# Kernel tuning notes

Hardware: AMD Instinct MI355X
Metric: run time of the kernel (lower is better)

The kernel has to match this reference:

```python
import jax, jax.numpy as jnp
import numpy as np

N_AREA = 10000
N_FEAT = 16
HID = 64
N_EDGE = 320000
BATCH = 64
EPS = 1e-5
SLOPE = 0.01  # F.leaky_relu default negative_slope


def _layer_norm(x, g, b):
    mu = jnp.mean(x, axis=-1, keepdims=True)
    var = jnp.mean(jnp.square(x - mu), axis=-1, keepdims=True)
    return (x - mu) * jax.lax.rsqrt(var + EPS) * g + b


def _leaky(x):
    return jnp.where(x >= 0, x, SLOPE * x)


def setup_inputs() -> dict:
    key = jax.random.key(0)
    ks = jax.random.split(key, 8)
    inp = {}
    inp["state"] = jax.random.normal(ks[0], (BATCH, N_AREA * N_FEAT), dtype=jnp.float32)
    inp["edge_index"] = jax.random.randint(ks[1], (2, N_EDGE), 0, N_AREA, dtype=jnp.int32)
    inp["batch_size"] = BATCH
    inp["rej_rate"] = jnp.zeros((1,), jnp.float32)
    inp["theta_value"] = jnp.zeros((1,), jnp.float32)
    inp["W1"] = jax.random.normal(ks[2], (N_FEAT, HID), jnp.float32) * 0.1
    inp["b1"] = jnp.zeros((HID,), jnp.float32)
    inp["W2"] = jax.random.normal(ks[3], (HID, HID), jnp.float32) * 0.1
    inp["b2"] = jnp.zeros((HID,), jnp.float32)
    inp["W3"] = jax.random.normal(ks[4], (HID, HID), jnp.float32) * 0.1
    inp["b3"] = jnp.zeros((HID,), jnp.float32)
    inp["g1"] = jnp.ones((HID,), jnp.float32)
    inp["be1"] = jnp.zeros((HID,), jnp.float32)
    inp["g3"] = jnp.ones((HID,), jnp.float32)
    inp["be3"] = jnp.zeros((HID,), jnp.float32)
    inp["Wf"] = jax.random.normal(ks[5], (HID, HID), jnp.float32) * 0.1
    inp["bf"] = jnp.zeros((HID,), jnp.float32)
    return inp


def reference(state, edge_index, batch_size, rej_rate, theta_value,
              W1, b1, W2, b2, W3, b3, g1, be1, g3, be3, Wf, bf):
    B = batch_size
    x = state.reshape(B, N_AREA, N_FEAT)
    # GCN normalization with self-loops (PyG GCNConv default)
    loops = jnp.arange(N_AREA, dtype=edge_index.dtype)
    src = jnp.concatenate([edge_index[0], loops])
    dst = jnp.concatenate([edge_index[1], loops])
    deg = jnp.zeros((N_AREA,), state.dtype).at[dst].add(1.0)
    dinv = jax.lax.rsqrt(jnp.maximum(deg, 1.0))  # deg >= 1 due to self-loops
    norm = dinv[src] * dinv[dst]  # [E+N]

    def conv(h, W, b):
        hw = h @ W                                  # [B, N, H]
        msg = hw[:, src, :] * norm[None, :, None]   # gather over sources
        out = jnp.zeros((B, N_AREA, W.shape[1]), hw.dtype).at[:, dst, :].add(msg)
        return out + b

    h1 = _leaky(_layer_norm(conv(x, W1, b1), g1, be1))
    h2 = _leaky(conv(h1, W2, b2)) + h1
    h3 = _leaky(_layer_norm(conv(h2, W3, b3), g3, be3)) + h1
    out = jnp.tanh(h3 @ Wf + bf)
    return out.reshape(B, -1)
```

## Files before the change

### kernel.cpp

```cpp
#include <hip/hip_runtime.h>
#include <hip/hip_fp16.h>
#include <cstdint>
#include <cstddef>

#define N_AREA 10000
#define N_FEAT 16
#define HID 64
#define BATCH 64
#define EPSL 1e-5f
#define SLOPE 0.01f
#define NCHUNK 157

typedef float fv4 __attribute__((ext_vector_type(4)));

__device__ __forceinline__ float lrelu(float x) { return x >= 0.f ? x : SLOPE * x; }
__device__ __forceinline__ float tanh_fast(float x) {
    float t = __expf(2.0f * x);
    return 1.0f - 2.0f / (t + 1.0f);
}
__device__ __forceinline__ float2 h2f2(unsigned u) {
    return __half22float2(*reinterpret_cast<const __half2*>(&u));
}
__device__ __forceinline__ unsigned f2h2(float a, float b) {
    __half2 h = __floats2half2_rn(a, b);
    return *reinterpret_cast<const unsigned*>(&h);
}
__device__ __forceinline__ fv4 cvt4(uint2 r) {
    float2 lo = h2f2(r.x), hi = h2f2(r.y);
    fv4 v = {lo.x, lo.y, hi.x, hi.y};
    return v;
}

__global__ __launch_bounds__(256) void k_zero(int* p, int n) {
    int i = blockIdx.x * 256 + threadIdx.x;
    if (i < n) p[i] = 0;
}

__global__ __launch_bounds__(256) void k_hist(const int* __restrict__ dst, int* __restrict__ counts, int E) {
    int e = blockIdx.x * 256 + threadIdx.x;
    if (e < E) atomicAdd(&counts[dst[e]], 1);
}

__global__ __launch_bounds__(1024) void k_scan(const int* __restrict__ counts, int* __restrict__ offsets,
                                               int* __restrict__ cursor, float* __restrict__ dinv,
                                               int2* __restrict__ ew) {
    const int PER = 10;
    int t = threadIdx.x;
    int base = t * PER;
    int local[PER];
    int sum = 0;
#pragma unroll
    for (int i = 0; i < PER; ++i) {
        int idx = base + i;
        int c = (idx < N_AREA) ? (((counts[idx] + 1) + 3) & ~3) : 0;
        local[i] = sum;
        sum += c;
    }
    __shared__ int part[1024];
    part[t] = sum;
    __syncthreads();
    for (int off = 1; off < 1024; off <<= 1) {
        int v = (t >= off) ? part[t - off] : 0;
        __syncthreads();
        part[t] += v;
        __syncthreads();
    }
    int excl = (t == 0) ? 0 : part[t - 1];
    if (t == 1023) {
        int tot = part[1023];
        offsets[N_AREA] = tot;
        for (int i = 0; i < 64; ++i) ew[tot + i] = make_int2(0, 0);
    }
    for (int i = 0; i < PER; ++i) {
        int idx = base + i;
        if (idx < N_AREA) {
            int off = excl + local[i];
            offsets[idx] = off;
            int c = counts[idx] + 1;
            int pc = (c + 3) & ~3;
            float dv = rsqrtf((float)c);
            dinv[idx] = dv;
            ew[off] = make_int2(idx, __float_as_int(dv * dv));
            for (int pp = c; pp < pc; ++pp) ew[off + pp] = make_int2(idx, 0);
            cursor[idx] = off + 1;
        }
    }
}

__global__ __launch_bounds__(256) void k_scatter(const int* __restrict__ ei, const float* __restrict__ dinv,
                                                 int* __restrict__ cursor, int2* __restrict__ ew, int E) {
    int e = blockIdx.x * 256 + threadIdx.x;
    if (e < E) {
        int s = ei[e], d = ei[E + e];
        int p = atomicAdd(&cursor[d], 1);
        ew[p] = make_int2(s, __float_as_int(dinv[s] * dinv[d]));
    }
}

__global__ __launch_bounds__(256, 8) void k_conv1(const float* __restrict__ state, const float* __restrict__ W1,
                                                  const float* __restrict__ b1, const float* __restrict__ g1,
                                                  const float* __restrict__ be1, unsigned short* __restrict__ h1,
                                                  const int* __restrict__ offs, const int2* __restrict__ ew) {
    __shared__ float xs[64][20];
    __shared__ float ws[16][64];
    int blk = blockIdx.x;
    int xc = blk & 7, ii = blk >> 3;
    int b = xc + 8 * (ii / NCHUNK);
    int c = ii % NCHUNK;
    int n0 = c * 64;
    int t = threadIdx.x;
    *(float4*)&ws[t >> 4][(t & 15) * 4] = *(const float4*)(W1 + (t >> 4) * HID + (t & 15) * 4);
    int ln = t >> 2, q = t & 3;
    int n = n0 + ln;
    const float* sb = state + (size_t)b * (N_AREA * N_FEAT);
    float4 acc = make_float4(0.f, 0.f, 0.f, 0.f);
    if (n < N_AREA) {
        int beg = offs[n], end = offs[n + 1];
        for (int e = beg; e < end; ++e) {
            int2 sw = ew[e];
            float w = __int_as_float(sw.y);
            float4 v = *(const float4*)(sb + (size_t)sw.x * N_FEAT + q * 4);
            acc.x += w * v.x; acc.y += w * v.y; acc.z += w * v.z; acc.w += w * v.w;
        }
    }
    *(float4*)&xs[ln][q * 4] = acc;
    __syncthreads();
    int wave = t >> 6, lane = t & 63;
    float bias = b1[lane], gg = g1[lane], bb = be1[lane];
    for (int j = 0; j < 16; ++j) {
        int lnn = wave * 16 + j;
        float a = bias;
#pragma unroll
        for (int f = 0; f < N_FEAT; ++f) a += xs[lnn][f] * ws[f][lane];
        float s = a;
#pragma unroll
        for (int m = 1; m < 64; m <<= 1) s += __shfl_xor(s, m);
        float mu = s * (1.0f / 64.0f);
        float dv = a - mu;
        float qv = dv * dv;
#pragma unroll
        for (int m = 1; m < 64; m <<= 1) qv += __shfl_xor(qv, m);
        float rstd = rsqrtf(qv * (1.0f / 64.0f) + EPSL);
        float y = lrelu(dv * rstd * gg + bb);
        int nn = n0 + lnn;
        unsigned hv = (unsigned)__half_as_ushort(__float2half_rn(y));
        unsigned ov = (unsigned)__shfl_xor((int)hv, 1);
        if (((lane & 1) == 0) && nn < N_AREA)
            *(unsigned*)(h1 + (size_t)b * (N_AREA * HID) + (size_t)nn * HID + lane) = hv | (ov << 16);
    }
}

template <int EPI>
__global__ __launch_bounds__(256, 8) void k_conv(const unsigned short* __restrict__ src, const float* __restrict__ W,
                                                 const float* __restrict__ bias, const float* __restrict__ g,
                                                 const float* __restrict__ be, const unsigned short* __restrict__ resid,
                                                 void* __restrict__ out, const int* __restrict__ offs,
                                                 const int2* __restrict__ ew, const float* __restrict__ Wf,
                                                 const float* __restrict__ bf) {
    __shared__ float a_t[64][68];
    int blk = blockIdx.x;
    int xc = blk & 7, ii = blk >> 3;
    int b = xc + 8 * (ii / NCHUNK);
    int c = ii % NCHUNK;
    int n0 = c * 64;
    int t = threadIdx.x;
    int lane = t & 63;
    int wave = __builtin_amdgcn_readfirstlane(t) >> 6;
    int q = lane >> 4;
    int ql = lane & 15;
    int f4 = ql * 4;
    const unsigned short* sp = src + (size_t)b * (N_AREA * HID);
    int nb = n0 + wave * 16;
    int beg = 0, end = 0;
    if (nb < N_AREA) { beg = offs[nb]; end = offs[nb + 1]; }
    int2 eC = ew[beg + lane];
    for (int j = 0; j < 16; ++j) {
        int n = nb + j;
        int cnt = (n < N_AREA) ? (end - beg) : 0;
        int nbeg = end;
        int nend = (n + 1 < N_AREA) ? offs[n + 2] : end;
        int2 eN = ew[nbeg + lane];
        int cmin = cnt > 64 ? 64 : cnt;
        fv4 a0 = {0.f, 0.f, 0.f, 0.f}, a1 = a0, a2 = a0, a3 = a0;
        int k16 = cmin >> 4;
        for (int k = 0; k < k16; ++k) {
            int s0 = 16 * k + q;
            int xa = __shfl(eC.x, s0),      wa = __shfl(eC.y, s0);
            int xb = __shfl(eC.x, s0 + 4),  wb = __shfl(eC.y, s0 + 4);
            int xc2 = __shfl(eC.x, s0 + 8), wc = __shfl(eC.y, s0 + 8);
            int xd = __shfl(eC.x, s0 + 12), wd = __shfl(eC.y, s0 + 12);
            uint2 ra = *(const uint2*)(sp + (unsigned)xa * HID + f4);
            uint2 rb = *(const uint2*)(sp + (unsigned)xb * HID + f4);
            uint2 rc = *(const uint2*)(sp + (unsigned)xc2 * HID + f4);
            uint2 rd = *(const uint2*)(sp + (unsigned)xd * HID + f4);
            a0 += __int_as_float(wa) * cvt4(ra);
            a1 += __int_as_float(wb) * cvt4(rb);
            a2 += __int_as_float(wc) * cvt4(rc);
            a3 += __int_as_float(wd) * cvt4(rd);
        }
        for (int e4 = k16 * 16; e4 < cmin; e4 += 4) {
            int sl = e4 + q;
            int xa = __shfl(eC.x, sl), wa = __shfl(eC.y, sl);
            uint2 ra = *(const uint2*)(sp + (unsigned)xa * HID + f4);
            a0 += __int_as_float(wa) * cvt4(ra);
        }
        if (cnt > 64) {
            for (int e = beg + 64; e < end; e += 4) {
                int2 ea = ew[e + q];
                uint2 ra = *(const uint2*)(sp + (unsigned)ea.x * HID + f4);
                a0 += __int_as_float(ea.y) * cvt4(ra);
            }
        }
        fv4 acc = (a0 + a1) + (a2 + a3);
        acc.x += __shfl_xor(acc.x, 16); acc.y += __shfl_xor(acc.y, 16);
        acc.z += __shfl_xor(acc.z, 16); acc.w += __shfl_xor(acc.w, 16);
        acc.x += __shfl_xor(acc.x, 32); acc.y += __shfl_xor(acc.y, 32);
        acc.z += __shfl_xor(acc.z, 32); acc.w += __shfl_xor(acc.w, 32);
        if (q == 0) {
            int ln = wave * 16 + j;
            int colp = 4 * ((ln >> 2) ^ (ql & 7)) + (ln & 3);
            a_t[f4 + 0][colp] = acc.x;
            a_t[f4 + 1][colp] = acc.y;
            a_t[f4 + 2][colp] = acc.z;
            a_t[f4 + 3][colp] = acc.w;
        }
        eC = eN; beg = nbeg; end = nend;
    }
    __syncthreads();
    int ty = t >> 4, tx = t & 15;
    int r0 = ty * 4, c0 = tx * 4;
    float am[4][4] = {};
#pragma unroll 4
    for (int k = 0; k < 64; ++k) {
        fv4 av = *(const fv4*)&a_t[k][4 * (ty ^ ((k >> 2) & 7))];
        float4 wv = *(const float4*)(W + k * HID + c0);
        am[0][0] += av.x * wv.x; am[0][1] += av.x * wv.y; am[0][2] += av.x * wv.z; am[0][3] += av.x * wv.w;
        am[1][0] += av.y * wv.x; am[1][1] += av.y * wv.y; am[1][2] += av.y * wv.z; am[1][3] += av.y * wv.w;
        am[2][0] += av.z * wv.x; am[2][1] += av.z * wv.y; am[2][2] += av.z * wv.z; am[2][3] += av.z * wv.w;
        am[3][0] += av.w * wv.x; am[3][1] += av.w * wv.y; am[3][2] += av.w * wv.z; am[3][3] += av.w * wv.w;
    }
    float4 bv = *(const float4*)(bias + c0);
#pragma unroll
    for (int i = 0; i < 4; ++i) {
        am[i][0] += bv.x; am[i][1] += bv.y; am[i][2] += bv.z; am[i][3] += bv.w;
    }
    if constexpr (EPI >= 1) {
        float4 gv = *(const float4*)(g + c0);
        float4 bev = *(const float4*)(be + c0);
        float gg[4] = {gv.x, gv.y, gv.z, gv.w};
        float bb[4] = {bev.x, bev.y, bev.z, bev.w};
#pragma unroll
        for (int i = 0; i < 4; ++i) {
            float s = am[i][0] + am[i][1] + am[i][2] + am[i][3];
            float qv = am[i][0] * am[i][0] + am[i][1] * am[i][1] + am[i][2] * am[i][2] + am[i][3] * am[i][3];
#pragma unroll
            for (int m = 1; m < 16; m <<= 1) {
                s += __shfl_xor(s, m);
                qv += __shfl_xor(qv, m);
            }
            float mu = s * (1.0f / 64.0f);
            float var = qv * (1.0f / 64.0f) - mu * mu;
            float rstd = rsqrtf(var + EPSL);
#pragma unroll
            for (int j = 0; j < 4; ++j) am[i][j] = (am[i][j] - mu) * rstd * gg[j] + bb[j];
        }
    }
    const unsigned short* rb = resid + (size_t)b * (N_AREA * HID);
    if constexpr (EPI == 0) {
        unsigned short* ob = (unsigned short*)out + (size_t)b * (N_AREA * HID);
#pragma unroll
        for (int i = 0; i < 4; ++i) {
            int n = n0 + r0 + i;
            if (n < N_AREA) {
                uint2 rr = *(const uint2*)(rb + (size_t)n * HID + c0);
                float2 r01 = h2f2(rr.x), r23 = h2f2(rr.y);
                float o0 = lrelu(am[i][0]) + r01.x;
                float o1 = lrelu(am[i][1]) + r01.y;
                float o2 = lrelu(am[i][2]) + r23.x;
                float o3 = lrelu(am[i][3]) + r23.y;
                uint2 st;
                st.x = f2h2(o0, o1);
                st.y = f2h2(o2, o3);
                *(uint2*)(ob + (size_t)n * HID + c0) = st;
            }
        }
    } else {
        float* ob = (float*)out + (size_t)b * (N_AREA * HID);
#pragma unroll
        for (int i = 0; i < 4; ++i) {
            int n = n0 + r0 + i;
            int nc = n < N_AREA ? n : (N_AREA - 1);
            uint2 rr = *(const uint2*)(rb + (size_t)nc * HID + c0);
            float2 r01 = h2f2(rr.x), r23 = h2f2(rr.y);
            am[i][0] = lrelu(am[i][0]) + r01.x;
            am[i][1] = lrelu(am[i][1]) + r01.y;
            am[i][2] = lrelu(am[i][2]) + r23.x;
            am[i][3] = lrelu(am[i][3]) + r23.y;
        }
        __syncthreads();
        float (*h3s)[68] = a_t;
#pragma unroll
        for (int i = 0; i < 4; ++i)
            *(float4*)&h3s[r0 + i][c0] = make_float4(am[i][0], am[i][1], am[i][2], am[i][3]);
        __syncthreads();
#pragma unroll
        for (int i = 0; i < 4; ++i) { am[i][0] = 0.f; am[i][1] = 0.f; am[i][2] = 0.f; am[i][3] = 0.f; }
#pragma unroll 4
        for (int k = 0; k < 64; ++k) {
            float4 wv = *(const float4*)(Wf + k * HID + c0);
            float a0 = h3s[r0 + 0][k];
            float a1 = h3s[r0 + 1][k];
            float a2 = h3s[r0 + 2][k];
            float a3 = h3s[r0 + 3][k];
            am[0][0] += a0 * wv.x; am[0][1] += a0 * wv.y; am[0][2] += a0 * wv.z; am[0][3] += a0 * wv.w;
            am[1][0] += a1 * wv.x; am[1][1] += a1 * wv.y; am[1][2] += a1 * wv.z; am[1][3] += a1 * wv.w;
            am[2][0] += a2 * wv.x; am[2][1] += a2 * wv.y; am[2][2] += a2 * wv.z; am[2][3] += a2 * wv.w;
            am[3][0] += a3 * wv.x; am[3][1] += a3 * wv.y; am[3][2] += a3 * wv.z; am[3][3] += a3 * wv.w;
        }
        float4 bfv = *(const float4*)(bf + c0);
#pragma unroll
        for (int i = 0; i < 4; ++i) {
            int n = n0 + r0 + i;
            if (n < N_AREA) {
                float4 o;
                o.x = tanh_fast(am[i][0] + bfv.x);
                o.y = tanh_fast(am[i][1] + bfv.y);
                o.z = tanh_fast(am[i][2] + bfv.z);
                o.w = tanh_fast(am[i][3] + bfv.w);
                *(float4*)(ob + (size_t)n * HID + c0) = o;
            }
        }
    }
}

extern "C" void kernel_launch(void* const* d_in, const int* in_sizes, int n_in,
                              void* d_out, int out_size, void* d_ws, size_t ws_size,
                              hipStream_t stream) {
    const float* state = (const float*)d_in[0];
    const int* ei = (const int*)d_in[1];
    const int E = in_sizes[1] / 2;
    const float* W1 = (const float*)d_in[5];
    const float* b1 = (const float*)d_in[6];
    const float* W2 = (const float*)d_in[7];
    const float* b2 = (const float*)d_in[8];
    const float* W3 = (const float*)d_in[9];
    const float* b3 = (const float*)d_in[10];
    const float* g1 = (const float*)d_in[11];
    const float* be1 = (const float*)d_in[12];
    const float* g3 = (const float*)d_in[13];
    const float* be3 = (const float*)d_in[14];
    const float* Wf = (const float*)d_in[15];
    const float* bf = (const float*)d_in[16];
    float* out = (float*)d_out;

    uint8_t* base = (uint8_t*)d_ws;
    size_t off = 0;
    auto carve = [&](size_t bytes) {
        void* p = base + off;
        off = (off + bytes + 255) & ~(size_t)255;
        return p;
    };
    float* dinv = (float*)carve(N_AREA * 4);
    int* counts = (int*)carve(N_AREA * 4);
    int* offsets = (int*)carve((N_AREA + 1) * 4);
    int* cursor = (int*)carve(N_AREA * 4);
    int2* ew = (int2*)carve(((size_t)E + 4 * N_AREA + 64) * 8);
    unsigned short* h1 = (unsigned short*)carve((size_t)BATCH * N_AREA * HID * 2);
    unsigned short* h2 = (unsigned short*)carve((size_t)BATCH * N_AREA * HID * 2);

    const int GRID = 8 * NCHUNK * (BATCH / 8);

    k_zero<<<(N_AREA + 255) / 256, 256, 0, stream>>>(counts, N_AREA);
    k_hist<<<(E + 255) / 256, 256, 0, stream>>>(ei + E, counts, E);
    k_scan<<<1, 1024, 0, stream>>>(counts, offsets, cursor, dinv, ew);
    k_scatter<<<(E + 255) / 256, 256, 0, stream>>>(ei, dinv, cursor, ew, E);

    k_conv1<<<GRID, 256, 0, stream>>>(state, W1, b1, g1, be1, h1, offsets, ew);
    k_conv<0><<<GRID, 256, 0, stream>>>(h1, W2, b2, nullptr, nullptr, h1, h2, offsets, ew, nullptr, nullptr);
    k_conv<2><<<GRID, 256, 0, stream>>>(h2, W3, b3, g3, be3, h1, out, offsets, ew, Wf, bf);
}
```

Before: 1.176 ms.

## Use fp16 MFMA for post-aggregation dense matmuls in conv kernels

```diff
diff --git a/kernel.cpp b/kernel.cpp
--- a/kernel.cpp
+++ b/kernel.cpp
@@ -12,6 +12,7 @@
 #define NCHUNK 157
 
 typedef float fv4 __attribute__((ext_vector_type(4)));
+typedef _Float16 h4 __attribute__((ext_vector_type(4)));
 
 __device__ __forceinline__ float lrelu(float x) { return x >= 0.f ? x : SLOPE * x; }
 __device__ __forceinline__ float tanh_fast(float x) {
@@ -30,6 +31,14 @@
     fv4 v = {lo.x, lo.y, hi.x, hi.y};
     return v;
 }
+__device__ __forceinline__ h4 pack4(float a, float b, float c, float d) {
+    auto p0 = __builtin_amdgcn_cvt_pkrtz(a, b);
+    auto p1 = __builtin_amdgcn_cvt_pkrtz(c, d);
+    h4 r;
+    *reinterpret_cast<decltype(p0)*>(&r) = p0;
+    *(reinterpret_cast<decltype(p0)*>(&r) + 1) = p1;
+    return r;
+}
 
 __global__ __launch_bounds__(256) void k_zero(int* p, int n) {
     int i = blockIdx.x * 256 + threadIdx.x;
@@ -39,6 +48,24 @@
 __global__ __launch_bounds__(256) void k_hist(const int* __restrict__ dst, int* __restrict__ counts, int E) {
     int e = blockIdx.x * 256 + threadIdx.x;
     if (e < E) atomicAdd(&counts[dst[e]], 1);
+}
+
+__global__ __launch_bounds__(256) void k_wcvt(const float* __restrict__ Wa, const float* __restrict__ Wb,
+                                              const float* __restrict__ Wc, _Float16* __restrict__ fa,
+                                              _Float16* __restrict__ fb, _Float16* __restrict__ fc) {
+    int t = threadIdx.x;
+    int lane = t & 63, pg = t >> 6;
+    int g = lane >> 4, q = lane & 15;
+    for (int p = pg; p < 16; p += 4) {
+        int mt = p >> 2, kk = p & 3;
+        int sb = (16 * kk + 4 * g) * HID + 16 * mt + q;
+        int dst = (p * 64 + lane) * 4;
+        for (int i = 0; i < 4; ++i) {
+            fa[dst + i] = (_Float16)Wa[sb + i * HID];
+            fb[dst + i] = (_Float16)Wb[sb + i * HID];
+            fc[dst + i] = (_Float16)Wc[sb + i * HID];
+        }
+    }
 }
 
 __global__ __launch_bounds__(1024) void k_scan(const int* __restrict__ counts, int* __restrict__ offsets,
@@ -151,11 +178,12 @@
 }
 
 template <int EPI>
-__global__ __launch_bounds__(256, 8) void k_conv(const unsigned short* __restrict__ src, const float* __restrict__ W,
+__global__ __launch_bounds__(256, 8) void k_conv(const unsigned short* __restrict__ src,
+                                                 const _Float16* __restrict__ Wfrag,
                                                  const float* __restrict__ bias, const float* __restrict__ g,
                                                  const float* __restrict__ be, const unsigned short* __restrict__ resid,
                                                  void* __restrict__ out, const int* __restrict__ offs,
-                                                 const int2* __restrict__ ew, const float* __restrict__ Wf,
+                                                 const int2* __restrict__ ew, const _Float16* __restrict__ WfFrag,
                                                  const float* __restrict__ bf) {
     __shared__ float a_t[64][68];
     int blk = blockIdx.x;
@@ -227,107 +255,105 @@
         eC = eN; beg = nbeg; end = nend;
     }
     __syncthreads();
-    int ty = t >> 4, tx = t & 15;
-    int r0 = ty * 4, c0 = tx * 4;
-    float am[4][4] = {};
-#pragma unroll 4
-    for (int k = 0; k < 64; ++k) {
-        fv4 av = *(const fv4*)&a_t[k][4 * (ty ^ ((k >> 2) & 7))];
-        float4 wv = *(const float4*)(W + k * HID + c0);
-        am[0][0] += av.x * wv.x; am[0][1] += av.x * wv.y; am[0][2] += av.x * wv.z; am[0][3] += av.x * wv.w;
-        am[1][0] += av.y * wv.x; am[1][1] += av.y * wv.y; am[1][2] += av.y * wv.z; am[1][3] += av.y * wv.w;
-        am[2][0] += av.z * wv.x; am[2][1] += av.z * wv.y; am[2][2] += av.z * wv.z; am[2][3] += av.z * wv.w;
-        am[3][0] += av.w * wv.x; am[3][1] += av.w * wv.y; am[3][2] += av.w * wv.z; am[3][3] += av.w * wv.w;
-    }
-    float4 bv = *(const float4*)(bias + c0);
-#pragma unroll
-    for (int i = 0; i < 4; ++i) {
-        am[i][0] += bv.x; am[i][1] += bv.y; am[i][2] += bv.z; am[i][3] += bv.w;
+    fv4 acc[4] = {{0.f, 0.f, 0.f, 0.f}, {0.f, 0.f, 0.f, 0.f}, {0.f, 0.f, 0.f, 0.f}, {0.f, 0.f, 0.f, 0.f}};
+#pragma unroll
+    for (int kk = 0; kk < 4; ++kk) {
+        int f0 = 16 * kk + 4 * q;
+        int colp = 4 * ((4 * wave + (ql >> 2)) ^ ((4 * kk + q) & 7)) + (ql & 3);
+        float b0 = a_t[f0 + 0][colp];
+        float b1 = a_t[f0 + 1][colp];
+        float b2 = a_t[f0 + 2][colp];
+        float b3 = a_t[f0 + 3][colp];
+        h4 bfr = pack4(b0, b1, b2, b3);
+#pragma unroll
+        for (int mt = 0; mt < 4; ++mt) {
+            h4 af = *(const h4*)(Wfrag + ((mt * 4 + kk) * 64 + lane) * 4);
+            acc[mt] = __builtin_amdgcn_mfma_f32_16x16x16f16(af, bfr, acc[mt], 0, 0, 0);
+        }
+    }
+    int nd = n0 + 16 * wave + ql;
+#pragma unroll
+    for (int mt = 0; mt < 4; ++mt) {
+        float4 bv = *(const float4*)(bias + 16 * mt + 4 * q);
+        acc[mt].x += bv.x; acc[mt].y += bv.y; acc[mt].z += bv.z; acc[mt].w += bv.w;
     }
     if constexpr (EPI >= 1) {
-        float4 gv = *(const float4*)(g + c0);
-        float4 bev = *(const float4*)(be + c0);
-        float gg[4] = {gv.x, gv.y, gv.z, gv.w};
-        float bb[4] = {bev.x, bev.y, bev.z, bev.w};
-#pragma unroll
-        for (int i = 0; i < 4; ++i) {
-            float s = am[i][0] + am[i][1] + am[i][2] + am[i][3];
-            float qv = am[i][0] * am[i][0] + am[i][1] * am[i][1] + am[i][2] * am[i][2] + am[i][3] * am[i][3];
-#pragma unroll
-            for (int m = 1; m < 16; m <<= 1) {
-                s += __shfl_xor(s, m);
-                qv += __shfl_xor(qv, m);
-            }
-            float mu = s * (1.0f / 64.0f);
-            float var = qv * (1.0f / 64.0f) - mu * mu;
-            float rstd = rsqrtf(var + EPSL);
-#pragma unroll
-            for (int j = 0; j < 4; ++j) am[i][j] = (am[i][j] - mu) * rstd * gg[j] + bb[j];
+        float s = 0.f, qv = 0.f;
+#pragma unroll
+        for (int mt = 0; mt < 4; ++mt) {
+            s += acc[mt].x + acc[mt].y + acc[mt].z + acc[mt].w;
+            qv += acc[mt].x * acc[mt].x + acc[mt].y * acc[mt].y + acc[mt].z * acc[mt].z + acc[mt].w * acc[mt].w;
+        }
+        s += __shfl_xor(s, 16); s += __shfl_xor(s, 32);
+        qv += __shfl_xor(qv, 16); qv += __shfl_xor(qv, 32);
+        float mu = s * (1.0f / 64.0f);
+        float var = qv * (1.0f / 64.0f) - mu * mu;
+        float rstd = rsqrtf(var + EPSL);
+#pragma unroll
+        for (int mt = 0; mt < 4; ++mt) {
+            float4 gv = *(const float4*)(g + 16 * mt + 4 * q);
+            float4 bev = *(const float4*)(be + 16 * mt + 4 * q);
+            acc[mt].x = (acc[mt].x - mu) * rstd * gv.x + bev.x;
+            acc[mt].y = (acc[mt].y - mu) * rstd * gv.y + bev.y;
+            acc[mt].z = (acc[mt].z - mu) * rstd * gv.z + bev.z;
+            acc[mt].w = (acc[mt].w - mu) * rstd * gv.w + bev.w;
         }
     }
     const unsigned short* rb = resid + (size_t)b * (N_AREA * HID);
     if constexpr (EPI == 0) {
         unsigned short* ob = (unsigned short*)out + (size_t)b * (N_AREA * HID);
-#pragma unroll
-        for (int i = 0; i < 4; ++i) {
-            int n = n0 + r0 + i;
-            if (n < N_AREA) {
-                uint2 rr = *(const uint2*)(rb + (size_t)n * HID + c0);
+        if (nd < N_AREA) {
+            size_t rowo = (size_t)nd * HID;
+#pragma unroll
+            for (int mt = 0; mt < 4; ++mt) {
+                int fo = 16 * mt + 4 * q;
+                uint2 rr = *(const uint2*)(rb + rowo + fo);
                 float2 r01 = h2f2(rr.x), r23 = h2f2(rr.y);
-                float o0 = lrelu(am[i][0]) + r01.x;
-                float o1 = lrelu(am[i][1]) + r01.y;
-                float o2 = lrelu(am[i][2]) + r23.x;
-                float o3 = lrelu(am[i][3]) + r23.y;
+                float o0 = lrelu(acc[mt].x) + r01.x;
+                float o1 = lrelu(acc[mt].y) + r01.y;
+                float o2 = lrelu(acc[mt].z) + r23.x;
+                float o3 = lrelu(acc[mt].w) + r23.y;
                 uint2 st;
                 st.x = f2h2(o0, o1);
                 st.y = f2h2(o2, o3);
-                *(uint2*)(ob + (size_t)n * HID + c0) = st;
+                *(uint2*)(ob + rowo + fo) = st;
             }
         }
     } else {
+        int ncl = nd < N_AREA ? nd : (N_AREA - 1);
+        size_t rowo = (size_t)ncl * HID;
+        h4 h3f[4];
+#pragma unroll
+        for (int mt = 0; mt < 4; ++mt) {
+            int fo = 16 * mt + 4 * q;
+            uint2 rr = *(const uint2*)(rb + rowo + fo);
+            float2 r01 = h2f2(rr.x), r23 = h2f2(rr.y);
+            float v0 = lrelu(acc[mt].x) + r01.x;
+            float v1 = lrelu(acc[mt].y) + r01.y;
+            float v2 = lrelu(acc[mt].z) + r23.x;
+            float v3 = lrelu(acc[mt].w) + r23.y;
+            h3f[mt] = pack4(v0, v1, v2, v3);
+        }
+        fv4 acc2[4] = {{0.f, 0.f, 0.f, 0.f}, {0.f, 0.f, 0.f, 0.f}, {0.f, 0.f, 0.f, 0.f}, {0.f, 0.f, 0.f, 0.f}};
+#pragma unroll
+        for (int kk = 0; kk < 4; ++kk) {
+#pragma unroll
+            for (int mt = 0; mt < 4; ++mt) {
+                h4 af = *(const h4*)(WfFrag + ((mt * 4 + kk) * 64 + lane) * 4);
+                acc2[mt] = __builtin_amdgcn_mfma_f32_16x16x16f16(af, h3f[kk], acc2[mt], 0, 0, 0);
+            }
+        }
         float* ob = (float*)out + (size_t)b * (N_AREA * HID);
-#pragma unroll
-        for (int i = 0; i < 4; ++i) {
-            int n = n0 + r0 + i;
-            int nc = n < N_AREA ? n : (N_AREA - 1);
-            uint2 rr = *(const uint2*)(rb + (size_t)nc * HID + c0);
-            float2 r01 = h2f2(rr.x), r23 = h2f2(rr.y);
-            am[i][0] = lrelu(am[i][0]) + r01.x;
-            am[i][1] = lrelu(am[i][1]) + r01.y;
-            am[i][2] = lrelu(am[i][2]) + r23.x;
-            am[i][3] = lrelu(am[i][3]) + r23.y;
-        }
-        __syncthreads();
-        float (*h3s)[68] = a_t;
-#pragma unroll
-        for (int i = 0; i < 4; ++i)
-            *(float4*)&h3s[r0 + i][c0] = make_float4(am[i][0], am[i][1], am[i][2], am[i][3]);
-        __syncthreads();
-#pragma unroll
-        for (int i = 0; i < 4; ++i) { am[i][0] = 0.f; am[i][1] = 0.f; am[i][2] = 0.f; am[i][3] = 0.f; }
-#pragma unroll 4
-        for (int k = 0; k < 64; ++k) {
-            float4 wv = *(const float4*)(Wf + k * HID + c0);
-            float a0 = h3s[r0 + 0][k];
-            float a1 = h3s[r0 + 1][k];
-            float a2 = h3s[r0 + 2][k];
-            float a3 = h3s[r0 + 3][k];
-            am[0][0] += a0 * wv.x; am[0][1] += a0 * wv.y; am[0][2] += a0 * wv.z; am[0][3] += a0 * wv.w;
-            am[1][0] += a1 * wv.x; am[1][1] += a1 * wv.y; am[1][2] += a1 * wv.z; am[1][3] += a1 * wv.w;
-            am[2][0] += a2 * wv.x; am[2][1] += a2 * wv.y; am[2][2] += a2 * wv.z; am[2][3] += a2 * wv.w;
-            am[3][0] += a3 * wv.x; am[3][1] += a3 * wv.y; am[3][2] += a3 * wv.z; am[3][3] += a3 * wv.w;
-        }
-        float4 bfv = *(const float4*)(bf + c0);
-#pragma unroll
-        for (int i = 0; i < 4; ++i) {
-            int n = n0 + r0 + i;
-            if (n < N_AREA) {
+        if (nd < N_AREA) {
+#pragma unroll
+            for (int mt = 0; mt < 4; ++mt) {
+                float4 bfv = *(const float4*)(bf + 16 * mt + 4 * q);
                 float4 o;
-                o.x = tanh_fast(am[i][0] + bfv.x);
-                o.y = tanh_fast(am[i][1] + bfv.y);
-                o.z = tanh_fast(am[i][2] + bfv.z);
-                o.w = tanh_fast(am[i][3] + bfv.w);
-                *(float4*)(ob + (size_t)n * HID + c0) = o;
+                o.x = tanh_fast(acc2[mt].x + bfv.x);
+                o.y = tanh_fast(acc2[mt].y + bfv.y);
+                o.z = tanh_fast(acc2[mt].z + bfv.z);
+                o.w = tanh_fast(acc2[mt].w + bfv.w);
+                *(float4*)(ob + (size_t)nd * HID + 16 * mt + 4 * q) = o;
             }
         }
     }
@@ -367,15 +393,19 @@
     int2* ew = (int2*)carve(((size_t)E + 4 * N_AREA + 64) * 8);
     unsigned short* h1 = (unsigned short*)carve((size_t)BATCH * N_AREA * HID * 2);
     unsigned short* h2 = (unsigned short*)carve((size_t)BATCH * N_AREA * HID * 2);
+    _Float16* w2f = (_Float16*)carve(4096 * 2);
+    _Float16* w3f = (_Float16*)carve(4096 * 2);
+    _Float16* wff = (_Float16*)carve(4096 * 2);
 
     const int GRID = 8 * NCHUNK * (BATCH / 8);
 
     k_zero<<<(N_AREA + 255) / 256, 256, 0, stream>>>(counts, N_AREA);
     k_hist<<<(E + 255) / 256, 256, 0, stream>>>(ei + E, counts, E);
+    k_wcvt<<<1, 256, 0, stream>>>(W2, W3, Wf, w2f, w3f, wff);
     k_scan<<<1, 1024, 0, stream>>>(counts, offsets, cursor, dinv, ew);
     k_scatter<<<(E + 255) / 256, 256, 0, stream>>>(ei, dinv, cursor, ew, E);
 
     k_conv1<<<GRID, 256, 0, stream>>>(state, W1, b1, g1, be1, h1, offsets, ew);
-    k_conv<0><<<GRID, 256, 0, stream>>>(h1, W2, b2, nullptr, nullptr, h1, h2, offsets, ew, nullptr, nullptr);
-    k_conv<2><<<GRID, 256, 0, stream>>>(h2, W3, b3, g3, be3, h1, out, offsets, ew, Wf, bf);
-}
+    k_conv<0><<<GRID, 256, 0, stream>>>(h1, w2f, b2, nullptr, nullptr, h1, h2, offsets, ew, nullptr, nullptr);
+    k_conv<2><<<GRID, 256, 0, stream>>>(h2, w3f, b3, g3, be3, h1, out, offsets, ew, wff, bf);
+}
```

New measurement: 1.059 ms. 1.11x faster.
